# Optimization experiments

Measured on AMD Instinct MI355X. Metric: run time of the kernel, lower is better.

## Reference

```python
import jax, jax.numpy as jnp
import numpy as np

IMG = 128      # raster_settings.image_size
FOCAL = 1.5    # simple pinhole projection (camera transform)
EPS = 1e-8
B, V, F = 4, 600, 1000


def setup_inputs() -> dict:
    key = jax.random.key(0)
    k1, k2 = jax.random.split(key)
    u = jax.random.uniform(k1, (B, V, 3), dtype=jnp.float32)
    xy = u[..., :2] * 2.0 - 1.0          # x,y in [-1, 1]
    z = u[..., 2:3] * 2.0 + 1.0          # z in [1, 3] (in front of camera)
    verts = jnp.concatenate([xy, z], axis=-1)   # [B, V, 3] world coords
    faces = jax.random.randint(k2, (F, 3), 0, V)  # [F, 3] vertex indices
    return {"verts": verts, "faces": faces}


def _pix_grid(H, W):
    # PyTorch3D NDC convention: +X left, +Y up; pixel centers at (2i+1)/S - 1 flipped.
    xs = 1.0 - (2.0 * jnp.arange(W, dtype=jnp.float32) + 1.0) / W
    ys = 1.0 - (2.0 * jnp.arange(H, dtype=jnp.float32) + 1.0) / H
    px = jnp.broadcast_to(xs[None, :], (H, W)).reshape(-1)  # [P]
    py = jnp.broadcast_to(ys[:, None], (H, W)).reshape(-1)  # [P]
    return px, py


def _edge(ax, ay, bx, by, px, py):
    # signed (twice-)area of triangle (a, b, p)
    return (bx - ax) * (py - ay) - (by - ay) * (px - ax)


def _seg_dist2(px, py, ax, ay, bx, by):
    # squared distance from point p to segment (a, b); all args broadcastable
    ex, ey = bx - ax, by - ay
    dx, dy = px - ax, py - ay
    ee = jnp.maximum(ex * ex + ey * ey, EPS)
    t = jnp.clip((dx * ex + dy * ey) / ee, 0.0, 1.0)
    rx = dx - t * ex
    ry = dy - t * ey
    return rx * rx + ry * ry


def _rasterize_one(v_ndc, faces, H, W):
    fv = v_ndc[faces]                       # [F, 3, 3] face vertices (ndc x, y, view z)
    v0, v1, v2 = fv[:, 0], fv[:, 1], fv[:, 2]
    px, py = _pix_grid(H, W)                # [P], P = H*W
    pxr, pyr = px[None, :], py[None, :]
    # signed face area [F]
    area = _edge(v0[:, 0], v0[:, 1], v1[:, 0], v1[:, 1], v2[:, 0], v2[:, 1])
    # edge functions at every pixel -> unnormalized barycentrics [F, P]
    w0 = _edge(v1[:, 0:1], v1[:, 1:2], v2[:, 0:1], v2[:, 1:2], pxr, pyr)
    w1 = _edge(v2[:, 0:1], v2[:, 1:2], v0[:, 0:1], v0[:, 1:2], pxr, pyr)
    w2 = _edge(v0[:, 0:1], v0[:, 1:2], v1[:, 0:1], v1[:, 1:2], pxr, pyr)
    denom = jnp.where(jnp.abs(area) > EPS, area, EPS)[:, None]
    s0, s1, s2 = w0 / denom, w1 / denom, w2 / denom
    zpix = s0 * v0[:, 2:3] + s1 * v1[:, 2:3] + s2 * v2[:, 2:3]  # [F, P]
    inside = (s0 >= 0) & (s1 >= 0) & (s2 >= 0) \
             & (jnp.abs(area)[:, None] > EPS) & (zpix > 0)
    zcand = jnp.where(inside, zpix, jnp.inf)
    idx = jnp.argmin(zcand, axis=0)                       # [P] winning face per pixel
    gather = lambda a: jnp.take_along_axis(a, idx[None, :], axis=0)[0]
    zmin = gather(zcand)
    hit = jnp.isfinite(zmin)
    b0, b1, b2 = gather(s0), gather(s1), gather(s2)       # winner barycentrics [P]
    # signed squared point-triangle distance at the winning face (negative inside)
    fw = fv[idx]                                          # [P, 3, 3]
    a, b, c = fw[:, 0], fw[:, 1], fw[:, 2]
    d2 = jnp.minimum(
        jnp.minimum(_seg_dist2(px, py, a[:, 0], a[:, 1], b[:, 0], b[:, 1]),
                    _seg_dist2(px, py, b[:, 0], b[:, 1], c[:, 0], c[:, 1])),
        _seg_dist2(px, py, c[:, 0], c[:, 1], a[:, 0], a[:, 1]))
    pix_to_face = jnp.where(hit, idx, -1).reshape(H, W)
    zbuf = jnp.where(hit, zmin, -1.0).reshape(H, W)
    bary = jnp.where(hit[:, None], jnp.stack([b0, b1, b2], -1), -1.0).reshape(H, W, 3)
    dists = jnp.where(hit, -d2, -1.0).reshape(H, W)
    return pix_to_face, zbuf, bary, dists


def reference(verts, faces):
    # camera transform: identity world-to-view, perspective projection, keep view z
    x = FOCAL * verts[..., 0] / verts[..., 2]
    y = FOCAL * verts[..., 1] / verts[..., 2]
    v_ndc = jnp.stack([x, y, verts[..., 2]], axis=-1)     # [B, V, 3]
    rast = lambda v: _rasterize_one(v, faces, IMG, IMG)
    pix_to_face, zbuf, bary, dists = jax.vmap(rast)(v_ndc)
    return pix_to_face, zbuf, bary, dists
```

## Files before the change

kernel.cpp:

```cpp
#include <hip/hip_runtime.h>
#include <math.h>

namespace {

constexpr int IMG  = 128;
constexpr int NPIX = IMG * IMG;
constexpr int B    = 4;
constexpr int V    = 600;
constexpr int F    = 1000;
constexpr int FP   = 1024;
constexpr float FOCALF = 1.5f;
constexpr float EPSF   = 1e-8f;
constexpr float EW   = 1e-4f;
constexpr float EBIN = 2e-4f;
constexpr float DENSAFE = 1e-3f;

__device__ inline float seg_dist2(float px, float py, float ax, float ay,
                                  float bx, float by) {
#pragma clang fp contract(off)
    float ex = bx - ax, ey = by - ay;
    float dx = px - ax, dy = py - ay;
    float ee = fmaxf(ex * ex + ey * ey, EPSF);
    float t  = (dx * ex + dy * ey) / ee;
    t = fminf(fmaxf(t, 0.0f), 1.0f);
    float rx = dx - t * ex;
    float ry = dy - t * ey;
    return rx * rx + ry * ry;
}

__global__ __launch_bounds__(256) void setup_clear(const float* __restrict__ verts,
                                                   const int* __restrict__ faces,
                                                   float* __restrict__ fdata,
                                                   unsigned long long* __restrict__ zbest) {
#pragma clang fp contract(off)
    int t = blockIdx.x * 256 + threadIdx.x;
    zbest[t] = ~0ULL;
    if (t >= B * FP) return;
    const int b = t >> 10, fp = t & (FP - 1);
    float* o = fdata + (size_t)t * 28;
    bool dead = (fp >= F);
    float e0x=0,e0y=0,bx=0,by=0,e1x=0,e1y=0,cx=0,cy=0,e2x=0,e2y=0,ax=0,ay=0;
    float den=0, z0=0, z1=0, z2=0;
    if (!dead) {
        int i0 = faces[fp * 3 + 0], i1 = faces[fp * 3 + 1], i2 = faces[fp * 3 + 2];
        const float* vb = verts + (size_t)b * V * 3;
        float x0 = vb[i0 * 3], y0 = vb[i0 * 3 + 1]; z0 = vb[i0 * 3 + 2];
        float x1 = vb[i1 * 3], y1 = vb[i1 * 3 + 1]; z1 = vb[i1 * 3 + 2];
        float x2 = vb[i2 * 3], y2 = vb[i2 * 3 + 1]; z2 = vb[i2 * 3 + 2];
        ax = (FOCALF * x0) / z0; ay = (FOCALF * y0) / z0;
        bx = (FOCALF * x1) / z1; by = (FOCALF * y1) / z1;
        cx = (FOCALF * x2) / z2; cy = (FOCALF * y2) / z2;
        e0x = cx - bx; e0y = cy - by;
        e1x = ax - cx; e1y = ay - cy;
        e2x = bx - ax; e2y = by - ay;
        den = e2x * (cy - ay) - e2y * (cx - ax);
        if (!(fabsf(den) > EPSF)) { den = 0.0f; dead = true; }
    }
    if (dead) {
        o[0] = 0.0f; o[1] = 0.0f; o[2] = -1e30f; o[3] = 0.0f;
        #pragma unroll
        for (int k = 4; k < 28; ++k) o[k] = 0.0f;
        return;
    }
    float a0 = -e0y, b0 = e0x, c0 = e0y * bx - e0x * by;
    float a1 = -e1y, b1 = e1x, c1 = e1y * cx - e1x * cy;
    float a2 = -e2y, b2 = e2x, c2 = e2y * ax - e2x * ay;
    const float s  = den > 0.0f ? 1.0f : -1.0f;
    const float rd = __builtin_amdgcn_rcpf(den);
    const float azr = z0 * rd, bzr = z1 * rd, czr = z2 * rd;
    const float Zx = a0 * azr + a1 * bzr + a2 * czr;
    const float Zy = b0 * azr + b1 * bzr + b2 * czr;
    const float Zc = c0 * azr + c1 * bzr + c2 * czr;
    const float S = (fabsf(a0) + fabsf(b0) + fabsf(c0)) * fabsf(azr)
                  + (fabsf(a1) + fabsf(b1) + fabsf(c1)) * fabsf(bzr)
                  + (fabsf(a2) + fabsf(b2) + fabsf(c2)) * fabsf(czr);
    const float eps = (fabsf(den) < DENSAFE) ? INFINITY : (1e-4f + 2e-6f * S);
    o[0]  = s * a0; o[1]  = s * b0; o[2]  = s * c0; o[3]  = s * den;
    o[4]  = s * a1; o[5]  = s * b1; o[6]  = s * c1; o[7]  = eps;
    o[8]  = Zx;     o[9]  = Zy;     o[10] = Zc;     o[11] = 0.0f;
    o[12] = e0x;    o[13] = e0y;    o[14] = bx;     o[15] = by;
    o[16] = e1x;    o[17] = e1y;    o[18] = cx;     o[19] = cy;
    o[20] = e2x;    o[21] = e2y;    o[22] = ax;     o[23] = ay;
    o[24] = den;    o[25] = z0;     o[26] = z1;     o[27] = z2;
}

__global__ __launch_bounds__(512, 8) void rast(const float* __restrict__ fdata,
                                               unsigned long long* __restrict__ zbest) {
#pragma clang fp contract(off)
    __shared__ float4 sface[64 * 7];
    __shared__ unsigned int lticket;
    const int tid  = threadIdx.x;
    const int lane = tid & 63;
    const int bk   = blockIdx.x;
    const int ch   = bk & 15;
    const int b    = (bk >> 4) & 3;
    const int slice = bk >> 6;
    if (tid == 0) lticket = 0u;

    const int f0 = ch * 64;
    const float4* gflat = (const float4*)(fdata + (size_t)(b * FP + f0) * 28);
    if (tid < 448) ((float4*)sface)[tid] = gflat[tid];

    const float4* fd4 = (const float4*)(fdata + (size_t)(b * FP + f0 + lane) * 28);
    const float4 m0 = fd4[0], m1 = fd4[1];
    const float a2s = -(m0.x + m1.x);
    const float b2s = -(m0.y + m1.y);
    const float c2s = m0.w - m0.z - m1.z;
    const bool c0x = m0.x >= 0.0f, c0y = m0.y >= 0.0f;
    const bool c1x = m1.x >= 0.0f, c1y = m1.y >= 0.0f;
    const bool c2x = a2s >= 0.0f, c2y = b2s >= 0.0f;
    __syncthreads();

    const int dpx = lane & 7, dpy = lane >> 3;

    for (;;) {
        unsigned int j = 0;
        if (lane == 0) j = atomicAdd(&lticket, 1u);
        j = (unsigned int)__shfl((int)j, 0);
        if (j >= 16u) break;
        const unsigned int jj = (j + (unsigned int)ch) & 15u;

        const int row = (slice >> 2) + 4 * (int)(jj >> 2);
        const int col = (slice & 3) + 4 * (int)(jj & 3);
        const int ix0 = col * 8, iy0 = row * 8;
        const int ix  = ix0 + dpx, iy = iy0 + dpy;
        const float px = 1.0f - (2.0f * (float)ix + 1.0f) / (float)IMG;
        const float py = 1.0f - (2.0f * (float)iy + 1.0f) / (float)IMG;
        const float pxmax = 1.0f - (2.0f * (float)ix0 + 1.0f) / (float)IMG;
        const float pxmin = 1.0f - (2.0f * (float)(ix0 + 7) + 1.0f) / (float)IMG;
        const float pymax = 1.0f - (2.0f * (float)iy0 + 1.0f) / (float)IMG;
        const float pymin = 1.0f - (2.0f * (float)(iy0 + 7) + 1.0f) / (float)IMG;

        const int gp = b * NPIX + iy * IMG + ix;
        const unsigned ztop = (unsigned)(zbest[gp] >> 32);
        float zbf = (ztop == 0xFFFFFFFFu) ? INFINITY : __uint_as_float(ztop);

        bool pass =
            (m0.x * (c0x ? pxmax : pxmin) + m0.y * (c0y ? pymax : pymin) + m0.z)
                >= -EBIN;
        pass &=
            (m1.x * (c1x ? pxmax : pxmin) + m1.y * (c1y ? pymax : pymin) + m1.z)
                >= -EBIN;
        pass &=
            (a2s * (c2x ? pxmax : pxmin) + b2s * (c2y ? pymax : pymin) + c2s)
                >= -EBIN;

        unsigned long long pmin = ~0ULL;
        unsigned long long mask = __ballot(pass);
        while (mask) {
            const int sl = __builtin_ctzll(mask);
            mask &= mask - 1;
            const float4 k0 = sface[sl * 7 + 0];
            const float4 k1 = sface[sl * 7 + 1];
            const float g0 = fmaf(k0.x, px, fmaf(k0.y, py, k0.z));
            const float g1 = fmaf(k1.x, px, fmaf(k1.y, py, k1.z));
            const float g2 = k0.w - g0 - g1;
            const bool maybe = (g0 >= -EW) & (g1 >= -EW) & (g2 >= -EW);
            if (!__any(maybe)) continue;
            const float4 kz = sface[sl * 7 + 2];
            const float zt = fmaf(kz.x, px, fmaf(kz.y, py, kz.z));
            const bool need = maybe & (zt < zbf + k1.w);
            if (__any(need)) {
                const float4 r0 = sface[sl * 7 + 3];
                const float4 r1 = sface[sl * 7 + 4];
                const float4 r2 = sface[sl * 7 + 5];
                const float4 r3 = sface[sl * 7 + 6];
                const float den = r3.x;
                float w0 = r0.x * (py - r0.w) - r0.y * (px - r0.z);
                float w1 = r1.x * (py - r1.w) - r1.y * (px - r1.z);
                float w2 = r2.x * (py - r2.w) - r2.y * (px - r2.z);
                const unsigned ds = __float_as_uint(den) >> 31;
                const bool in0 = (w0 == 0.0f) | ((__float_as_uint(w0) >> 31) == ds);
                const bool in1 = (w1 == 0.0f) | ((__float_as_uint(w1) >> 31) == ds);
                const bool in2 = (w2 == 0.0f) | ((__float_as_uint(w2) >> 31) == ds);
                if (in0 & in1 & in2) {
                    float s0 = w0 / den, s1 = w1 / den, s2 = w2 / den;
                    float z  = s0 * r3.y + s1 * r3.z + s2 * r3.w;
                    if (z > 0.0f) {
                        unsigned long long pk =
                            ((unsigned long long)__float_as_uint(z) << 32) |
                            (unsigned)(f0 + sl);
                        pmin = pmin < pk ? pmin : pk;
                        zbf  = fminf(zbf, z);
                    }
                }
            }
        }
        if (pmin != ~0ULL) atomicMin(&zbest[gp], pmin);
    }
}

__global__ __launch_bounds__(256) void pass2(const float* __restrict__ fdata,
                                             const unsigned long long* __restrict__ zbest,
                                             float* __restrict__ out) {
#pragma clang fp contract(off)
    const int gp = blockIdx.x * 256 + threadIdx.x;
    const int b  = gp >> 14;
    const int p  = gp & (NPIX - 1);
    const int ix = p & (IMG - 1), iy = p >> 7;

    unsigned long long packed = zbest[gp];
    float o_face = -1.0f, o_z = -1.0f, o_b0 = -1.0f, o_b1 = -1.0f,
          o_b2 = -1.0f, o_d = -1.0f;

    if (packed != ~0ULL) {
        const int   idx = (int)(unsigned)(packed & 0xffffffffu);
        const float z   = __uint_as_float((unsigned)(packed >> 32));
        const float px  = 1.0f - (2.0f * (float)ix + 1.0f) / (float)IMG;
        const float py  = 1.0f - (2.0f * (float)iy + 1.0f) / (float)IMG;

        const float4* fd4 = (const float4*)(fdata + (size_t)(b * FP + idx) * 28);
        float4 q0 = fd4[3], q1 = fd4[4], q2 = fd4[5], q3 = fd4[6];
        float den = q3.x;
        float w0 = q0.x * (py - q0.w) - q0.y * (px - q0.z);
        float w1 = q1.x * (py - q1.w) - q1.y * (px - q1.z);
        float w2 = q2.x * (py - q2.w) - q2.y * (px - q2.z);
        float s0 = w0 / den, s1 = w1 / den, s2 = w2 / den;

        float d2 = fminf(fminf(seg_dist2(px, py, q2.z, q2.w, q0.z, q0.w),
                               seg_dist2(px, py, q0.z, q0.w, q1.z, q1.w)),
                         seg_dist2(px, py, q1.z, q1.w, q2.z, q2.w));
        o_face = (float)idx; o_z = z;
        o_b0 = s0; o_b1 = s1; o_b2 = s2;
        o_d = -d2;
    }

    out[gp]            = o_face;
    out[B * NPIX + gp] = o_z;
    const int bary_base = 2 * B * NPIX;
    out[bary_base + gp * 3 + 0] = o_b0;
    out[bary_base + gp * 3 + 1] = o_b1;
    out[bary_base + gp * 3 + 2] = o_b2;
    out[5 * B * NPIX + gp] = o_d;
}

}

extern "C" void kernel_launch(void* const* d_in, const int* in_sizes, int n_in,
                              void* d_out, int out_size, void* d_ws, size_t ws_size,
                              hipStream_t stream) {
    const float* verts = (const float*)d_in[0];
    const int*   faces = (const int*)d_in[1];
    float* out = (float*)d_out;

    char* ws = (char*)d_ws;
    unsigned long long* zbest = (unsigned long long*)ws;
    float* fdata = (float*)(ws + (size_t)B * NPIX * 8);

    setup_clear<<<B * NPIX / 256, 256, 0, stream>>>(verts, faces, fdata, zbest);
    rast<<<1024, 512, 0, stream>>>(fdata, zbest);
    pass2<<<B * NPIX / 256, 256, 0, stream>>>(fdata, zbest, out);
}
```

Baseline: 31.42 us.

## Fuse face setup into raster and pass2, replace setup kernel with memset

Removes the separate setup kernel that precomputed per-face records in global memory. Each raster block now projects its 64 faces directly into shared memory, and pass2 re-projects the winning face from the vertices. The zbuf clear becomes a hipMemsetAsync. This drops one kernel's global writes and reads and its dependency, at the cost of recomputing face setup in all 1024 raster blocks and issuing scattered vertex gathers per pixel in pass2.

```diff
diff --git a/kernel.cpp b/kernel.cpp
--- a/kernel.cpp
+++ b/kernel.cpp
@@ -8,12 +8,38 @@
 constexpr int B    = 4;
 constexpr int V    = 600;
 constexpr int F    = 1000;
-constexpr int FP   = 1024;
 constexpr float FOCALF = 1.5f;
 constexpr float EPSF   = 1e-8f;
 constexpr float EW   = 1e-4f;
 constexpr float EBIN = 2e-4f;
 constexpr float DENSAFE = 1e-3f;
+
+struct FaceRec {
+    float e0x, e0y, bx, by;
+    float e1x, e1y, cx, cy;
+    float e2x, e2y, ax, ay;
+    float den, z0, z1, z2;
+};
+
+__device__ inline FaceRec project_face(const float* __restrict__ vb,
+                                       const int* __restrict__ faces, int f) {
+#pragma clang fp contract(off)
+    FaceRec r;
+    int i0 = faces[f * 3 + 0], i1 = faces[f * 3 + 1], i2 = faces[f * 3 + 2];
+    float x0 = vb[i0 * 3], y0 = vb[i0 * 3 + 1]; r.z0 = vb[i0 * 3 + 2];
+    float x1 = vb[i1 * 3], y1 = vb[i1 * 3 + 1]; r.z1 = vb[i1 * 3 + 2];
+    float x2 = vb[i2 * 3], y2 = vb[i2 * 3 + 1]; r.z2 = vb[i2 * 3 + 2];
+    r.ax = (FOCALF * x0) / r.z0; r.ay = (FOCALF * y0) / r.z0;
+    r.bx = (FOCALF * x1) / r.z1; r.by = (FOCALF * y1) / r.z1;
+    r.cx = (FOCALF * x2) / r.z2; r.cy = (FOCALF * y2) / r.z2;
+    r.e0x = r.cx - r.bx; r.e0y = r.cy - r.by;
+    r.e1x = r.ax - r.cx; r.e1y = r.ay - r.cy;
+    r.e2x = r.bx - r.ax; r.e2y = r.by - r.ay;
+    float den = r.e2x * (r.cy - r.ay) - r.e2y * (r.cx - r.ax);
+    if (!(fabsf(den) > EPSF)) den = 0.0f;
+    r.den = den;
+    return r;
+}
 
 __device__ inline float seg_dist2(float px, float py, float ax, float ay,
                                   float bx, float by) {
@@ -28,63 +54,8 @@
     return rx * rx + ry * ry;
 }
 
-__global__ __launch_bounds__(256) void setup_clear(const float* __restrict__ verts,
-                                                   const int* __restrict__ faces,
-                                                   float* __restrict__ fdata,
-                                                   unsigned long long* __restrict__ zbest) {
-#pragma clang fp contract(off)
-    int t = blockIdx.x * 256 + threadIdx.x;
-    zbest[t] = ~0ULL;
-    if (t >= B * FP) return;
-    const int b = t >> 10, fp = t & (FP - 1);
-    float* o = fdata + (size_t)t * 28;
-    bool dead = (fp >= F);
-    float e0x=0,e0y=0,bx=0,by=0,e1x=0,e1y=0,cx=0,cy=0,e2x=0,e2y=0,ax=0,ay=0;
-    float den=0, z0=0, z1=0, z2=0;
-    if (!dead) {
-        int i0 = faces[fp * 3 + 0], i1 = faces[fp * 3 + 1], i2 = faces[fp * 3 + 2];
-        const float* vb = verts + (size_t)b * V * 3;
-        float x0 = vb[i0 * 3], y0 = vb[i0 * 3 + 1]; z0 = vb[i0 * 3 + 2];
-        float x1 = vb[i1 * 3], y1 = vb[i1 * 3 + 1]; z1 = vb[i1 * 3 + 2];
-        float x2 = vb[i2 * 3], y2 = vb[i2 * 3 + 1]; z2 = vb[i2 * 3 + 2];
-        ax = (FOCALF * x0) / z0; ay = (FOCALF * y0) / z0;
-        bx = (FOCALF * x1) / z1; by = (FOCALF * y1) / z1;
-        cx = (FOCALF * x2) / z2; cy = (FOCALF * y2) / z2;
-        e0x = cx - bx; e0y = cy - by;
-        e1x = ax - cx; e1y = ay - cy;
-        e2x = bx - ax; e2y = by - ay;
-        den = e2x * (cy - ay) - e2y * (cx - ax);
-        if (!(fabsf(den) > EPSF)) { den = 0.0f; dead = true; }
-    }
-    if (dead) {
-        o[0] = 0.0f; o[1] = 0.0f; o[2] = -1e30f; o[3] = 0.0f;
-        #pragma unroll
-        for (int k = 4; k < 28; ++k) o[k] = 0.0f;
-        return;
-    }
-    float a0 = -e0y, b0 = e0x, c0 = e0y * bx - e0x * by;
-    float a1 = -e1y, b1 = e1x, c1 = e1y * cx - e1x * cy;
-    float a2 = -e2y, b2 = e2x, c2 = e2y * ax - e2x * ay;
-    const float s  = den > 0.0f ? 1.0f : -1.0f;
-    const float rd = __builtin_amdgcn_rcpf(den);
-    const float azr = z0 * rd, bzr = z1 * rd, czr = z2 * rd;
-    const float Zx = a0 * azr + a1 * bzr + a2 * czr;
-    const float Zy = b0 * azr + b1 * bzr + b2 * czr;
-    const float Zc = c0 * azr + c1 * bzr + c2 * czr;
-    const float S = (fabsf(a0) + fabsf(b0) + fabsf(c0)) * fabsf(azr)
-                  + (fabsf(a1) + fabsf(b1) + fabsf(c1)) * fabsf(bzr)
-                  + (fabsf(a2) + fabsf(b2) + fabsf(c2)) * fabsf(czr);
-    const float eps = (fabsf(den) < DENSAFE) ? INFINITY : (1e-4f + 2e-6f * S);
-    o[0]  = s * a0; o[1]  = s * b0; o[2]  = s * c0; o[3]  = s * den;
-    o[4]  = s * a1; o[5]  = s * b1; o[6]  = s * c1; o[7]  = eps;
-    o[8]  = Zx;     o[9]  = Zy;     o[10] = Zc;     o[11] = 0.0f;
-    o[12] = e0x;    o[13] = e0y;    o[14] = bx;     o[15] = by;
-    o[16] = e1x;    o[17] = e1y;    o[18] = cx;     o[19] = cy;
-    o[20] = e2x;    o[21] = e2y;    o[22] = ax;     o[23] = ay;
-    o[24] = den;    o[25] = z0;     o[26] = z1;     o[27] = z2;
-}
-
-__global__ __launch_bounds__(512, 8) void rast(const float* __restrict__ fdata,
+__global__ __launch_bounds__(512, 8) void rast(const float* __restrict__ verts,
+                                               const int* __restrict__ faces,
                                                unsigned long long* __restrict__ zbest) {
 #pragma clang fp contract(off)
     __shared__ float4 sface[64 * 7];
@@ -97,20 +68,57 @@
     const int slice = bk >> 6;
     if (tid == 0) lticket = 0u;
 
-    const int f0 = ch * 64;
-    const float4* gflat = (const float4*)(fdata + (size_t)(b * FP + f0) * 28);
-    if (tid < 448) ((float4*)sface)[tid] = gflat[tid];
-
-    const float4* fd4 = (const float4*)(fdata + (size_t)(b * FP + f0 + lane) * 28);
-    const float4 m0 = fd4[0], m1 = fd4[1];
+    if (tid < 64) {
+        const int fid = ch * 64 + tid;
+        float4 o0, o1, o2, o3, o4, o5, o6;
+        bool dead = (fid >= F);
+        FaceRec r = {};
+        if (!dead) {
+            r = project_face(verts + (size_t)b * V * 3, faces, fid);
+            dead = (r.den == 0.0f);
+        }
+        if (dead) {
+            o0 = make_float4(0.0f, 0.0f, -1e30f, 0.0f);
+            o1 = make_float4(0.0f, 0.0f, -1e30f, 0.0f);
+            o2 = make_float4(0.0f, 0.0f, 0.0f, 0.0f);
+            o3 = o4 = o5 = o6 = make_float4(0.0f, 0.0f, 0.0f, 0.0f);
+        } else {
+            float a0 = -r.e0y, b0 = r.e0x, c0 = r.e0y * r.bx - r.e0x * r.by;
+            float a1 = -r.e1y, b1 = r.e1x, c1 = r.e1y * r.cx - r.e1x * r.cy;
+            float a2 = -r.e2y, b2 = r.e2x, c2 = r.e2y * r.ax - r.e2x * r.ay;
+            const float s  = r.den > 0.0f ? 1.0f : -1.0f;
+            const float rd = __builtin_amdgcn_rcpf(r.den);
+            const float azr = r.z0 * rd, bzr = r.z1 * rd, czr = r.z2 * rd;
+            const float Zx = a0 * azr + a1 * bzr + a2 * czr;
+            const float Zy = b0 * azr + b1 * bzr + b2 * czr;
+            const float Zc = c0 * azr + c1 * bzr + c2 * czr;
+            const float S = (fabsf(a0) + fabsf(b0) + fabsf(c0)) * fabsf(azr)
+                          + (fabsf(a1) + fabsf(b1) + fabsf(c1)) * fabsf(bzr)
+                          + (fabsf(a2) + fabsf(b2) + fabsf(c2)) * fabsf(czr);
+            const float eps = (fabsf(r.den) < DENSAFE) ? INFINITY
+                                                       : (1e-4f + 2e-6f * S);
+            o0 = make_float4(s * a0, s * b0, s * c0, s * r.den);
+            o1 = make_float4(s * a1, s * b1, s * c1, eps);
+            o2 = make_float4(Zx, Zy, Zc, 0.0f);
+            o3 = make_float4(r.e0x, r.e0y, r.bx, r.by);
+            o4 = make_float4(r.e1x, r.e1y, r.cx, r.cy);
+            o5 = make_float4(r.e2x, r.e2y, r.ax, r.ay);
+            o6 = make_float4(r.den, r.z0, r.z1, r.z2);
+        }
+        float4* o = &sface[tid * 7];
+        o[0] = o0; o[1] = o1; o[2] = o2; o[3] = o3; o[4] = o4; o[5] = o5; o[6] = o6;
+    }
+    __syncthreads();
+
+    const float4 m0 = sface[lane * 7 + 0], m1 = sface[lane * 7 + 1];
     const float a2s = -(m0.x + m1.x);
     const float b2s = -(m0.y + m1.y);
     const float c2s = m0.w - m0.z - m1.z;
     const bool c0x = m0.x >= 0.0f, c0y = m0.y >= 0.0f;
     const bool c1x = m1.x >= 0.0f, c1y = m1.y >= 0.0f;
     const bool c2x = a2s >= 0.0f, c2y = b2s >= 0.0f;
-    __syncthreads();
-
+
+    const int f0 = ch * 64;
     const int dpx = lane & 7, dpy = lane >> 3;
 
     for (;;) {
@@ -190,7 +198,8 @@
     }
 }
 
-__global__ __launch_bounds__(256) void pass2(const float* __restrict__ fdata,
+__global__ __launch_bounds__(256) void pass2(const float* __restrict__ verts,
+                                             const int* __restrict__ faces,
                                              const unsigned long long* __restrict__ zbest,
                                              float* __restrict__ out) {
 #pragma clang fp contract(off)
@@ -209,17 +218,15 @@
         const float px  = 1.0f - (2.0f * (float)ix + 1.0f) / (float)IMG;
         const float py  = 1.0f - (2.0f * (float)iy + 1.0f) / (float)IMG;
 
-        const float4* fd4 = (const float4*)(fdata + (size_t)(b * FP + idx) * 28);
-        float4 q0 = fd4[3], q1 = fd4[4], q2 = fd4[5], q3 = fd4[6];
-        float den = q3.x;
-        float w0 = q0.x * (py - q0.w) - q0.y * (px - q0.z);
-        float w1 = q1.x * (py - q1.w) - q1.y * (px - q1.z);
-        float w2 = q2.x * (py - q2.w) - q2.y * (px - q2.z);
-        float s0 = w0 / den, s1 = w1 / den, s2 = w2 / den;
-
-        float d2 = fminf(fminf(seg_dist2(px, py, q2.z, q2.w, q0.z, q0.w),
-                               seg_dist2(px, py, q0.z, q0.w, q1.z, q1.w)),
-                         seg_dist2(px, py, q1.z, q1.w, q2.z, q2.w));
+        FaceRec r = project_face(verts + (size_t)b * V * 3, faces, idx);
+        float w0 = r.e0x * (py - r.by) - r.e0y * (px - r.bx);
+        float w1 = r.e1x * (py - r.cy) - r.e1y * (px - r.cx);
+        float w2 = r.e2x * (py - r.ay) - r.e2y * (px - r.ax);
+        float s0 = w0 / r.den, s1 = w1 / r.den, s2 = w2 / r.den;
+
+        float d2 = fminf(fminf(seg_dist2(px, py, r.ax, r.ay, r.bx, r.by),
+                               seg_dist2(px, py, r.bx, r.by, r.cx, r.cy)),
+                         seg_dist2(px, py, r.cx, r.cy, r.ax, r.ay));
         o_face = (float)idx; o_z = z;
         o_b0 = s0; o_b1 = s1; o_b2 = s2;
         o_d = -d2;
@@ -243,11 +250,9 @@
     const int*   faces = (const int*)d_in[1];
     float* out = (float*)d_out;
 
-    char* ws = (char*)d_ws;
-    unsigned long long* zbest = (unsigned long long*)ws;
-    float* fdata = (float*)(ws + (size_t)B * NPIX * 8);
-
-    setup_clear<<<B * NPIX / 256, 256, 0, stream>>>(verts, faces, fdata, zbest);
-    rast<<<1024, 512, 0, stream>>>(fdata, zbest);
-    pass2<<<B * NPIX / 256, 256, 0, stream>>>(fdata, zbest, out);
-}
+    unsigned long long* zbest = (unsigned long long*)d_ws;
+
+    hipMemsetAsync(zbest, 0xFF, (size_t)B * NPIX * 8, stream);
+    rast<<<1024, 512, 0, stream>>>(verts, faces, zbest);
+    pass2<<<B * NPIX / 256, 256, 0, stream>>>(verts, faces, zbest, out);
+}
```

New measurement: 32.36 us. 3.0% more time.
